# Performance work log

Measured on AMD Instinct MI355X. Metric: run time of the kernel, lower is better.

## Reference

```python
import jax, jax.numpy as jnp
import numpy as np
from jax import lax

WIN = 11
NUM_CLASSES = 2
WEIGHTS = (1.0, 0.5)
PAD = (WIN - 1) // 2


def _edge_kernel():
    w = -jnp.ones((1, 1, WIN, WIN), jnp.float32)
    return w.at[0, 0, WIN // 2, WIN // 2].set(WIN * WIN - 1.0)


def setup_inputs() -> dict:
    key = jax.random.key(0)
    k0, k1, k2 = jax.random.split(key, 3)
    B, H, W = 16, 1024, 1024
    score0 = jax.random.normal(k0, (B, NUM_CLASSES, H, W), jnp.float32)
    score1 = jax.random.normal(k1, (B, NUM_CLASSES, H, W), jnp.float32)
    target = jax.random.randint(k2, (B, 1, H, W), 0, NUM_CLASSES, jnp.int32)
    return {"score0": score0, "score1": score1, "target": target}


def _loss_one(x, onehot, edge_mask, smoothing):
    # x: [B,C,H,W] logits; onehot: [B,C,H,W]; edge_mask: [B,1,H,W]
    log_p = jax.nn.log_softmax(x, axis=1)
    alpha = smoothing
    # softlabel: filled with alpha, target class gets 1 - alpha + alpha/C
    soft = alpha + onehot * (1.0 - 2.0 * alpha + alpha / NUM_CLASSES)
    mask = onehot * (1.0 - edge_mask) + soft * edge_mask
    # sum over class dim, mean over (B,H,W), negated
    return -jnp.mean(jnp.sum(mask * log_p, axis=1))


def reference(score0, score1, target):
    tgt_f = target.astype(jnp.float32)  # [B,1,H,W]
    edge = lax.conv_general_dilated(
        tgt_f, _edge_kernel(), window_strides=(1, 1),
        padding=((PAD, PAD), (PAD, PAD)),
        dimension_numbers=("NCHW", "OIHW", "NCHW"))
    edge_mask = (edge != 0).astype(jnp.float32)          # [B,1,H,W]
    smoothing = jnp.minimum(jnp.mean(edge_mask), 0.2)
    cls = jnp.arange(NUM_CLASSES, dtype=jnp.int32).reshape(1, NUM_CLASSES, 1, 1)
    onehot = (target == cls).astype(jnp.float32)         # [B,C,H,W]
    loss = (WEIGHTS[0] * _loss_one(score0, onehot, edge_mask, smoothing)
            + WEIGHTS[1] * _loss_one(score1, onehot, edge_mask, smoothing))
    return loss
```

## Files before the change

kernel.cpp:

```cpp
#include <hip/hip_runtime.h>

#define TW   128
#define TH   32
#define HALO 5
#define TIW  (TW + 2*HALO)
#define TIH  (TH + 2*HALO)
#define TB_P 144
#define VS_P 142
#define NBX  8
#define NBY  32
#define NBZ  16
#define NB   (NBX*NBY*NBZ)
#define NPIX 16777216.0

__global__ __launch_bounds__(256)
void fused_edge_loss(const float* __restrict__ score0,
                     const float* __restrict__ score1,
                     const int*   __restrict__ target,
                     float*       __restrict__ ws) {
    __shared__ unsigned char  tb[TIH][TB_P];
    __shared__ unsigned short vs[TH][VS_P];
    __shared__ float          red[4][5];

    const int tid   = threadIdx.x;
    const int tileX = blockIdx.x * TW;
    const int tileY = blockIdx.y * TH;
    const int b     = blockIdx.z;
    const int bid   = (blockIdx.z * NBY + blockIdx.y) * NBX + blockIdx.x;

    const int* tgt = target + (size_t)b * (1024 * 1024);

    for (int idx = tid; idx < TIH * TIW; idx += 256) {
        int rr = idx / TIW;
        int cc = idx - rr * TIW;
        int gr = tileY + rr - HALO;
        int gc = tileX + cc - HALO;
        unsigned char v = 0;
        if ((unsigned)gr < 1024u && (unsigned)gc < 1024u)
            v = (unsigned char)tgt[gr * 1024 + gc];
        tb[rr][cc] = v;
    }
    __syncthreads();

    if (tid < TIW) {
        int acc = 0;
        #pragma unroll
        for (int rr = 0; rr < 11; ++rr) acc += tb[rr][tid];
        vs[0][tid] = (unsigned short)acc;
        for (int r = 1; r < TH; ++r) {
            acc += (int)tb[r + 10][tid] - (int)tb[r - 1][tid];
            vs[r][tid] = (unsigned short)acc;
        }
    }
    __syncthreads();

    const float* s0b = score0 + (size_t)b * (2 * 1024 * 1024);
    const float* s1b = score1 + (size_t)b * (2 * 1024 * 1024);
    const int tx = tid & 31;
    const int ty = tid >> 5;

    float cnt = 0.f, a1 = 0.f, a2 = 0.f, b1 = 0.f, b2 = 0.f;

    #pragma unroll
    for (int p = 0; p < 4; ++p) {
        const int r  = ty + p * 8;
        const int gr = tileY + r;
        const int c0 = tx * 4;
        const int gc = tileX + c0;

        int S[4];
        int s = 0;
        #pragma unroll
        for (int k = 0; k < 11; ++k) s += vs[r][c0 + k];
        S[0] = s;
        #pragma unroll
        for (int j = 1; j < 4; ++j) {
            s += (int)vs[r][c0 + 10 + j] - (int)vs[r][c0 + j - 1];
            S[j] = s;
        }

        const size_t base = (size_t)gr * 1024 + gc;
        float4 x0 = *(const float4*)(s0b + base);
        float4 x1 = *(const float4*)(s0b + 1048576 + base);
        float4 y0 = *(const float4*)(s1b + base);
        float4 y1 = *(const float4*)(s1b + 1048576 + base);
        float p0a[4] = {x0.x, x0.y, x0.z, x0.w};
        float p1a[4] = {x1.x, x1.y, x1.z, x1.w};
        float q0a[4] = {y0.x, y0.y, y0.z, y0.w};
        float q1a[4] = {y1.x, y1.y, y1.z, y1.w};

        #pragma unroll
        for (int j = 0; j < 4; ++j) {
            const int t = tb[r + 5][c0 + 5 + j];
            const float e = (S[j] != 121 * t) ? 1.0f : 0.0f;
            cnt += e;

            {
                float p0 = p0a[j], p1 = p1a[j];
                float m   = fmaxf(p0, p1);
                float lse = m + __logf(1.0f + __expf(-fabsf(p0 - p1)));
                float lpt = (t ? p1 : p0) - lse;
                float slp = p0 + p1 - 2.0f * lse;
                a1 += lpt;
                a2 += e * (slp - 1.5f * lpt);
            }
            {
                float q0 = q0a[j], q1 = q1a[j];
                float m   = fmaxf(q0, q1);
                float lse = m + __logf(1.0f + __expf(-fabsf(q0 - q1)));
                float lpt = (t ? q1 : q0) - lse;
                float slp = q0 + q1 - 2.0f * lse;
                b1 += lpt;
                b2 += e * (slp - 1.5f * lpt);
            }
        }
    }

    float vals[5] = {cnt, a1, a2, b1, b2};
    const int lane = tid & 63, wv = tid >> 6;
    #pragma unroll
    for (int q = 0; q < 5; ++q) {
        float v = vals[q];
        #pragma unroll
        for (int off = 32; off > 0; off >>= 1) v += __shfl_down(v, off);
        if (lane == 0) red[wv][q] = v;
    }
    __syncthreads();
    if (tid == 0) {
        #pragma unroll
        for (int q = 0; q < 5; ++q) {
            float v = red[0][q] + red[1][q] + red[2][q] + red[3][q];
            ws[q * NB + bid] = v;
        }
    }
}

__global__ __launch_bounds__(256)
void finalize_loss(const float* __restrict__ ws, float* __restrict__ out) {
    __shared__ double red[4][5];
    const int tid = threadIdx.x;
    double acc[5] = {0, 0, 0, 0, 0};
    for (int i = tid; i < NB; i += 256) {
        #pragma unroll
        for (int q = 0; q < 5; ++q) acc[q] += (double)ws[q * NB + i];
    }
    const int lane = tid & 63, wv = tid >> 6;
    #pragma unroll
    for (int q = 0; q < 5; ++q) {
        double v = acc[q];
        #pragma unroll
        for (int off = 32; off > 0; off >>= 1) v += __shfl_down(v, off);
        if (lane == 0) red[wv][q] = v;
    }
    __syncthreads();
    if (tid == 0) {
        double s[5];
        #pragma unroll
        for (int q = 0; q < 5; ++q)
            s[q] = red[0][q] + red[1][q] + red[2][q] + red[3][q];
        const double N = NPIX;
        double alpha = s[0] / N;
        if (alpha > 0.2) alpha = 0.2;
        double loss = (s[1] + alpha * s[2]) + 0.5 * (s[3] + alpha * s[4]);
        out[0] = (float)(-loss / N);
    }
}

extern "C" void kernel_launch(void* const* d_in, const int* in_sizes, int n_in,
                              void* d_out, int out_size, void* d_ws, size_t ws_size,
                              hipStream_t stream) {
    const float* score0 = (const float*)d_in[0];
    const float* score1 = (const float*)d_in[1];
    const int*   target = (const int*)d_in[2];
    float* out = (float*)d_out;
    float* ws  = (float*)d_ws;

    dim3 grid(NBX, NBY, NBZ);
    fused_edge_loss<<<grid, 256, 0, stream>>>(score0, score1, target, ws);
    finalize_loss<<<1, 256, 0, stream>>>(ws, out);
}
```

Measured before the change: 343.4 us.

## Split edge detection into packed-mask pass and separate streaming loss kernel

Splits the fused kernel into two. The first computes the edge mask and target bits and packs them into one byte per 4 pixels, along with per-block edge counts. The second is a grid-stride loss kernel with 2048 blocks that streams the score tensors with 8 pixels per thread, decoupling the bandwidth-heavy loads from the shared-memory box-filter stage. This costs an extra launch plus a 4 MB packed buffer write and read, and the old fused path is kept as a fallback when the workspace is too small.

```diff
diff --git a/kernel.cpp b/kernel.cpp
--- a/kernel.cpp
+++ b/kernel.cpp
@@ -1,4 +1,9 @@
 #include <hip/hip_runtime.h>
+
+#define HW_SZ   (1024*1024)
+#define NPIX    16777216.0
+#define GROUPS  (16*1024*1024/4)
+#define PAIRS   (GROUPS/2)
 
 #define TW   128
 #define TH   32
@@ -10,17 +15,20 @@
 #define NBX  8
 #define NBY  32
 #define NBZ  16
-#define NB   (NBX*NBY*NBZ)
-#define NPIX 16777216.0
-
-__global__ __launch_bounds__(256)
-void fused_edge_loss(const float* __restrict__ score0,
-                     const float* __restrict__ score1,
-                     const int*   __restrict__ target,
-                     float*       __restrict__ ws) {
+#define NB1  (NBX*NBY*NBZ)
+
+#define NB2  2048
+
+#define PACKED_BYTES (GROUPS)
+#define WS_NEEDED (PACKED_BYTES + NB1*4 + 4*NB2*4)
+
+__global__ __launch_bounds__(256)
+void edge_pack(const int* __restrict__ target,
+               unsigned char* __restrict__ packed,
+               float* __restrict__ cntpart) {
     __shared__ unsigned char  tb[TIH][TB_P];
     __shared__ unsigned short vs[TH][VS_P];
-    __shared__ float          red[4][5];
+    __shared__ float          red[4];
 
     const int tid   = threadIdx.x;
     const int tileX = blockIdx.x * TW;
@@ -28,7 +36,7 @@
     const int b     = blockIdx.z;
     const int bid   = (blockIdx.z * NBY + blockIdx.y) * NBX + blockIdx.x;
 
-    const int* tgt = target + (size_t)b * (1024 * 1024);
+    const int* tgt = target + (size_t)b * HW_SZ;
 
     for (int idx = tid; idx < TIH * TIW; idx += 256) {
         int rr = idx / TIW;
@@ -54,8 +62,189 @@
     }
     __syncthreads();
 
-    const float* s0b = score0 + (size_t)b * (2 * 1024 * 1024);
-    const float* s1b = score1 + (size_t)b * (2 * 1024 * 1024);
+    const int tx = tid & 31;
+    const int ty = tid >> 5;
+
+    int cnt = 0;
+    #pragma unroll
+    for (int p = 0; p < 4; ++p) {
+        const int r  = ty + p * 8;
+        const int gr = tileY + r;
+        const int c0 = tx * 4;
+
+        int S[4];
+        int s = 0;
+        #pragma unroll
+        for (int k = 0; k < 11; ++k) s += vs[r][c0 + k];
+        S[0] = s;
+        #pragma unroll
+        for (int j = 1; j < 4; ++j) {
+            s += (int)vs[r][c0 + 10 + j] - (int)vs[r][c0 + j - 1];
+            S[j] = s;
+        }
+
+        unsigned int pk = 0;
+        #pragma unroll
+        for (int j = 0; j < 4; ++j) {
+            const int t = tb[r + 5][c0 + 5 + j];
+            const int e = (S[j] != 121 * t) ? 1 : 0;
+            cnt += e;
+            pk |= (unsigned)(t << (2 * j)) | (unsigned)(e << (2 * j + 1));
+        }
+        packed[((size_t)b << 18) + (gr << 8) + (tileX >> 2) + tx] = (unsigned char)pk;
+    }
+
+    float v = (float)cnt;
+    #pragma unroll
+    for (int off = 32; off > 0; off >>= 1) v += __shfl_down(v, off);
+    const int lane = tid & 63, wv = tid >> 6;
+    if (lane == 0) red[wv] = v;
+    __syncthreads();
+    if (tid == 0) cntpart[bid] = red[0] + red[1] + red[2] + red[3];
+}
+
+__device__ __forceinline__ void px_term(float p0, float p1, int t, float e,
+                                        float& s1, float& s2) {
+    float m   = fmaxf(p0, p1);
+    float lse = m + __logf(1.0f + __expf(-fabsf(p0 - p1)));
+    float lpt = (t ? p1 : p0) - lse;
+    float slp = p0 + p1 - 2.0f * lse;
+    s1 += lpt;
+    s2 += e * (slp - 1.5f * lpt);
+}
+
+__global__ __launch_bounds__(256)
+void loss_stream(const float* __restrict__ score0,
+                 const float* __restrict__ score1,
+                 const unsigned char* __restrict__ packed,
+                 float* __restrict__ spart) {
+    const int tid = threadIdx.x;
+    const unsigned short* pk16 = (const unsigned short*)packed;
+
+    float a1 = 0.f, a2 = 0.f, b1 = 0.f, b2 = 0.f;
+
+    for (int pp = blockIdx.x * 256 + tid; pp < PAIRS; pp += NB2 * 256) {
+        const int b = pp >> 17;
+        const size_t off = ((size_t)pp << 3) + ((size_t)b << 20);
+
+        float4 x0a = *(const float4*)(score0 + off);
+        float4 x0b = *(const float4*)(score0 + off + 4);
+        float4 x1a = *(const float4*)(score0 + off + HW_SZ);
+        float4 x1b = *(const float4*)(score0 + off + HW_SZ + 4);
+        float4 y0a = *(const float4*)(score1 + off);
+        float4 y0b = *(const float4*)(score1 + off + 4);
+        float4 y1a = *(const float4*)(score1 + off + HW_SZ);
+        float4 y1b = *(const float4*)(score1 + off + HW_SZ + 4);
+        const unsigned int pk = pk16[pp];
+
+        float p0[8] = {x0a.x, x0a.y, x0a.z, x0a.w, x0b.x, x0b.y, x0b.z, x0b.w};
+        float p1[8] = {x1a.x, x1a.y, x1a.z, x1a.w, x1b.x, x1b.y, x1b.z, x1b.w};
+        float q0[8] = {y0a.x, y0a.y, y0a.z, y0a.w, y0b.x, y0b.y, y0b.z, y0b.w};
+        float q1[8] = {y1a.x, y1a.y, y1a.z, y1a.w, y1b.x, y1b.y, y1b.z, y1b.w};
+
+        #pragma unroll
+        for (int j = 0; j < 8; ++j) {
+            const int   t = (pk >> (2 * j)) & 1;
+            const float e = (float)((pk >> (2 * j + 1)) & 1);
+            px_term(p0[j], p1[j], t, e, a1, a2);
+            px_term(q0[j], q1[j], t, e, b1, b2);
+        }
+    }
+
+    __shared__ float red[4][4];
+    float vals[4] = {a1, a2, b1, b2};
+    const int lane = tid & 63, wv = tid >> 6;
+    #pragma unroll
+    for (int q = 0; q < 4; ++q) {
+        float v = vals[q];
+        #pragma unroll
+        for (int off = 32; off > 0; off >>= 1) v += __shfl_down(v, off);
+        if (lane == 0) red[wv][q] = v;
+    }
+    __syncthreads();
+    if (tid == 0) {
+        #pragma unroll
+        for (int q = 0; q < 4; ++q)
+            spart[q * NB2 + blockIdx.x] = red[0][q] + red[1][q] + red[2][q] + red[3][q];
+    }
+}
+
+__global__ __launch_bounds__(256)
+void finalize2(const float* __restrict__ cntpart,
+               const float* __restrict__ spart,
+               float* __restrict__ out) {
+    __shared__ double red[4][5];
+    const int tid = threadIdx.x;
+    double acc[5] = {0, 0, 0, 0, 0};
+    for (int i = tid; i < NB1; i += 256) acc[0] += (double)cntpart[i];
+    for (int i = tid; i < NB2; i += 256) {
+        #pragma unroll
+        for (int q = 0; q < 4; ++q) acc[q + 1] += (double)spart[q * NB2 + i];
+    }
+    const int lane = tid & 63, wv = tid >> 6;
+    #pragma unroll
+    for (int q = 0; q < 5; ++q) {
+        double v = acc[q];
+        #pragma unroll
+        for (int off = 32; off > 0; off >>= 1) v += __shfl_down(v, off);
+        if (lane == 0) red[wv][q] = v;
+    }
+    __syncthreads();
+    if (tid == 0) {
+        double s[5];
+        #pragma unroll
+        for (int q = 0; q < 5; ++q)
+            s[q] = red[0][q] + red[1][q] + red[2][q] + red[3][q];
+        double alpha = s[0] / NPIX;
+        if (alpha > 0.2) alpha = 0.2;
+        double loss = (s[1] + alpha * s[2]) + 0.5 * (s[3] + alpha * s[4]);
+        out[0] = (float)(-loss / NPIX);
+    }
+}
+
+__global__ __launch_bounds__(256)
+void fused_edge_loss(const float* __restrict__ score0,
+                     const float* __restrict__ score1,
+                     const int*   __restrict__ target,
+                     float*       __restrict__ ws) {
+    __shared__ unsigned char  tb[TIH][TB_P];
+    __shared__ unsigned short vs[TH][VS_P];
+    __shared__ float          red[4][5];
+
+    const int tid   = threadIdx.x;
+    const int tileX = blockIdx.x * TW;
+    const int tileY = blockIdx.y * TH;
+    const int b     = blockIdx.z;
+    const int bid   = (blockIdx.z * NBY + blockIdx.y) * NBX + blockIdx.x;
+
+    const int* tgt = target + (size_t)b * HW_SZ;
+
+    for (int idx = tid; idx < TIH * TIW; idx += 256) {
+        int rr = idx / TIW;
+        int cc = idx - rr * TIW;
+        int gr = tileY + rr - HALO;
+        int gc = tileX + cc - HALO;
+        unsigned char v = 0;
+        if ((unsigned)gr < 1024u && (unsigned)gc < 1024u)
+            v = (unsigned char)tgt[gr * 1024 + gc];
+        tb[rr][cc] = v;
+    }
+    __syncthreads();
+
+    if (tid < TIW) {
+        int acc = 0;
+        #pragma unroll
+        for (int rr = 0; rr < 11; ++rr) acc += tb[rr][tid];
+        vs[0][tid] = (unsigned short)acc;
+        for (int r = 1; r < TH; ++r) {
+            acc += (int)tb[r + 10][tid] - (int)tb[r - 1][tid];
+            vs[r][tid] = (unsigned short)acc;
+        }
+    }
+    __syncthreads();
+
+    const float* s0b = score0 + (size_t)b * (2 * HW_SZ);
+    const float* s1b = score1 + (size_t)b * (2 * HW_SZ);
     const int tx = tid & 31;
     const int ty = tid >> 5;
 
@@ -81,9 +270,9 @@
 
         const size_t base = (size_t)gr * 1024 + gc;
         float4 x0 = *(const float4*)(s0b + base);
-        float4 x1 = *(const float4*)(s0b + 1048576 + base);
+        float4 x1 = *(const float4*)(s0b + HW_SZ + base);
         float4 y0 = *(const float4*)(s1b + base);
-        float4 y1 = *(const float4*)(s1b + 1048576 + base);
+        float4 y1 = *(const float4*)(s1b + HW_SZ + base);
         float p0a[4] = {x0.x, x0.y, x0.z, x0.w};
         float p1a[4] = {x1.x, x1.y, x1.z, x1.w};
         float q0a[4] = {y0.x, y0.y, y0.z, y0.w};
@@ -94,25 +283,8 @@
             const int t = tb[r + 5][c0 + 5 + j];
             const float e = (S[j] != 121 * t) ? 1.0f : 0.0f;
             cnt += e;
-
-            {
-                float p0 = p0a[j], p1 = p1a[j];
-                float m   = fmaxf(p0, p1);
-                float lse = m + __logf(1.0f + __expf(-fabsf(p0 - p1)));
-                float lpt = (t ? p1 : p0) - lse;
-                float slp = p0 + p1 - 2.0f * lse;
-                a1 += lpt;
-                a2 += e * (slp - 1.5f * lpt);
-            }
-            {
-                float q0 = q0a[j], q1 = q1a[j];
-                float m   = fmaxf(q0, q1);
-                float lse = m + __logf(1.0f + __expf(-fabsf(q0 - q1)));
-                float lpt = (t ? q1 : q0) - lse;
-                float slp = q0 + q1 - 2.0f * lse;
-                b1 += lpt;
-                b2 += e * (slp - 1.5f * lpt);
-            }
+            px_term(p0a[j], p1a[j], t, e, a1, a2);
+            px_term(q0a[j], q1a[j], t, e, b1, b2);
         }
     }
 
@@ -128,10 +300,8 @@
     __syncthreads();
     if (tid == 0) {
         #pragma unroll
-        for (int q = 0; q < 5; ++q) {
-            float v = red[0][q] + red[1][q] + red[2][q] + red[3][q];
-            ws[q * NB + bid] = v;
-        }
+        for (int q = 0; q < 5; ++q)
+            ws[q * NB1 + bid] = red[0][q] + red[1][q] + red[2][q] + red[3][q];
     }
 }
 
@@ -140,9 +310,9 @@
     __shared__ double red[4][5];
     const int tid = threadIdx.x;
     double acc[5] = {0, 0, 0, 0, 0};
-    for (int i = tid; i < NB; i += 256) {
-        #pragma unroll
-        for (int q = 0; q < 5; ++q) acc[q] += (double)ws[q * NB + i];
+    for (int i = tid; i < NB1; i += 256) {
+        #pragma unroll
+        for (int q = 0; q < 5; ++q) acc[q] += (double)ws[q * NB1 + i];
     }
     const int lane = tid & 63, wv = tid >> 6;
     #pragma unroll
@@ -158,11 +328,10 @@
         #pragma unroll
         for (int q = 0; q < 5; ++q)
             s[q] = red[0][q] + red[1][q] + red[2][q] + red[3][q];
-        const double N = NPIX;
-        double alpha = s[0] / N;
+        double alpha = s[0] / NPIX;
         if (alpha > 0.2) alpha = 0.2;
         double loss = (s[1] + alpha * s[2]) + 0.5 * (s[3] + alpha * s[4]);
-        out[0] = (float)(-loss / N);
+        out[0] = (float)(-loss / NPIX);
     }
 }
 
@@ -173,9 +342,20 @@
     const float* score1 = (const float*)d_in[1];
     const int*   target = (const int*)d_in[2];
     float* out = (float*)d_out;
-    float* ws  = (float*)d_ws;
-
-    dim3 grid(NBX, NBY, NBZ);
-    fused_edge_loss<<<grid, 256, 0, stream>>>(score0, score1, target, ws);
-    finalize_loss<<<1, 256, 0, stream>>>(ws, out);
-}
+
+    if (ws_size >= (size_t)WS_NEEDED) {
+        unsigned char* packed  = (unsigned char*)d_ws;
+        float*         cntpart = (float*)((char*)d_ws + PACKED_BYTES);
+        float*         spart   = cntpart + NB1;
+
+        dim3 grid1(NBX, NBY, NBZ);
+        edge_pack<<<grid1, 256, 0, stream>>>(target, packed, cntpart);
+        loss_stream<<<NB2, 256, 0, stream>>>(score0, score1, packed, spart);
+        finalize2<<<1, 256, 0, stream>>>(cntpart, spart, out);
+    } else {
+        float* ws = (float*)d_ws;
+        dim3 grid(NBX, NBY, NBZ);
+        fused_edge_loss<<<grid, 256, 0, stream>>>(score0, score1, target, ws);
+        finalize_loss<<<1, 256, 0, stream>>>(ws, out);
+    }
+}
```

New measurement: 348.2 us. Within noise of the previous version (+1.4%).
